# Kernel tuning notes

Measured on AMD Instinct MI355X. Metric: run time of the kernel, lower is better.

## Reference

```python
import jax, jax.numpy as jnp
import numpy as np

C_M = 256
C = 32
C_Z = 128
EPS = 1e-5


def setup_inputs() -> dict:
    key = jax.random.key(0)
    ks = jax.random.split(key, 8)
    b, s, i = 1, 128, 256
    msa = jax.random.normal(ks[0], (b, s, i, C_M), dtype=jnp.float32)
    scale_in = 1.0 / np.sqrt(C_M)
    scale_out = 1.0 / np.sqrt(C * C)
    return {
        "msa_representation": msa,
        "ln_w": jnp.ones((C_M,), jnp.float32),
        "ln_b": jnp.zeros((C_M,), jnp.float32),
        "w_left": jax.random.normal(ks[1], (C_M, C), jnp.float32) * scale_in,
        "b_left": jax.random.normal(ks[2], (C,), jnp.float32) * scale_in,
        "w_right": jax.random.normal(ks[3], (C_M, C), jnp.float32) * scale_in,
        "b_right": jax.random.normal(ks[4], (C,), jnp.float32) * scale_in,
        "w_out": jax.random.normal(ks[5], (C * C, C_Z), jnp.float32) * scale_out,
        "b_out": jax.random.normal(ks[6], (C_Z,), jnp.float32) * scale_out,
    }


def reference(msa_representation, ln_w, ln_b, w_left, b_left, w_right, b_right, w_out, b_out):
    x = msa_representation
    # LayerNorm over c_m
    mu = jnp.mean(x, axis=-1, keepdims=True)
    var = jnp.mean(jnp.square(x - mu), axis=-1, keepdims=True)
    x = (x - mu) * jax.lax.rsqrt(var + EPS) * ln_w + ln_b
    # dual projections: [b, s, i, c]
    A = x @ w_left + b_left
    B = x @ w_right + b_right
    s_dim = x.shape[1]
    # outer product mean over MSA depth s: [b, i, j, c, c]
    outer = jnp.einsum('bsic,bsjd->bijcd', A, B) / s_dim
    b_, i_, j_ = outer.shape[0], outer.shape[1], outer.shape[2]
    flat = outer.reshape(b_, i_, j_, C * C)
    return flat @ w_out + b_out
```

## Files before the change

### kernel.cpp

```cpp
#include <hip/hip_runtime.h>

typedef __attribute__((ext_vector_type(8))) short short8;
typedef __attribute__((ext_vector_type(4))) float f32x4;

#define CM 256
#define CC 32
#define CZ 128
#define SDIM 128
#define IDIM 256

__device__ __forceinline__ unsigned short f2bf(float f) {
  union { float f; unsigned u; } v; v.f = f;
  unsigned r = v.u + 0x7fffu + ((v.u >> 16) & 1u);
  return (unsigned short)(r >> 16);
}
__device__ __forceinline__ unsigned pack_bf2(float a, float b) {
  union { float f; unsigned u; } x, y; x.f = a; y.f = b;
  return ((x.u + 0x8000u) >> 16) | ((y.u + 0x8000u) & 0xffff0000u);
}

__global__ void k_prep(const float* __restrict__ wl, const float* __restrict__ wr,
                       const float* __restrict__ wo,
                       unsigned short* __restrict__ wlrT, unsigned short* __restrict__ WF) {
  int t = blockIdx.x * 256 + threadIdx.x;
  if (t < 64 * 256) {
    int c = t >> 8, e = t & 255;
    float v = (c < CC) ? wl[e * CC + c] : wr[e * CC + (c - CC)];
    wlrT[c * 256 + e] = f2bf(v);
  } else {
    int t2 = t - 64 * 256;
    if (t2 < 8 * 32 * 64) {
      int zt = t2 >> 11, ks = (t2 >> 6) & 31, lane = t2 & 63;
      int ln = lane & 15, qd = lane >> 4;
      int z = zt * 16 + ln;
#pragma unroll
      for (int e = 0; e < 8; ++e) {
        int c = qd * 8 + e, d = ks;
        WF[(size_t)t2 * 8 + e] = f2bf(wo[(c * 32 + d) * CZ + z] * (1.0f / 128.0f));
      }
    }
  }
}

__global__ __launch_bounds__(512) void k_lnproj(
    const float* __restrict__ x, const float* __restrict__ lnw, const float* __restrict__ lnb,
    const float* __restrict__ bl, const float* __restrict__ br,
    const unsigned short* __restrict__ wlrT,
    unsigned short* __restrict__ A2, unsigned short* __restrict__ Bbuf) {
  extern __shared__ __align__(16) char lds[];
  unsigned short* xn = (unsigned short*)lds;
  unsigned short* sT = (unsigned short*)(lds + 67584);
  int tid = threadIdx.x;
  int lane = tid & 63, ww = tid >> 6;
  int qd = lane >> 4, ln = lane & 15;
  int i = blockIdx.x;

  for (int rr = 0; rr < 16; ++rr) {
    int s = ww * 16 + rr;
    float4 v = ((const float4*)(x + ((size_t)s * IDIM + i) * CM))[lane];
    float s1 = v.x + v.y + v.z + v.w;
    float s2 = v.x * v.x + v.y * v.y + v.z * v.z + v.w * v.w;
#pragma unroll
    for (int off = 32; off; off >>= 1) {
      s1 += __shfl_xor(s1, off);
      s2 += __shfl_xor(s2, off);
    }
    float mu = s1 * (1.0f / 256.0f);
    float var = s2 * (1.0f / 256.0f) - mu * mu;
    float rs = rsqrtf(var + 1e-5f);
    float4 w4 = ((const float4*)lnw)[lane];
    float4 b4 = ((const float4*)lnb)[lane];
    ushort4 h;
    h.x = f2bf((v.x - mu) * rs * w4.x + b4.x);
    h.y = f2bf((v.y - mu) * rs * w4.y + b4.y);
    h.z = f2bf((v.z - mu) * rs * w4.z + b4.z);
    h.w = f2bf((v.w - mu) * rs * w4.w + b4.w);
    *(ushort4*)&xn[s * 264 + lane * 4] = h;
  }
  __syncthreads();

  f32x4 acc[4];
#pragma unroll
  for (int nt = 0; nt < 4; ++nt) acc[nt] = (f32x4){0.f, 0.f, 0.f, 0.f};
#pragma unroll
  for (int ks = 0; ks < 8; ++ks) {
    short8 af = *(const short8*)&xn[(ww * 16 + ln) * 264 + ks * 32 + qd * 8];
#pragma unroll
    for (int nt = 0; nt < 4; ++nt) {
      short8 bf = *(const short8*)(wlrT + (nt * 16 + ln) * 256 + ks * 32 + qd * 8);
      acc[nt] = __builtin_amdgcn_mfma_f32_16x16x32_bf16(af, bf, acc[nt], 0, 0, 0);
    }
  }
#pragma unroll
  for (int nt = 0; nt < 4; ++nt) {
    int c64 = nt * 16 + ln;
    float bias = (c64 < CC) ? bl[c64] : br[c64 - CC];
    ushort4 h;
    h.x = f2bf(acc[nt][0] + bias);
    h.y = f2bf(acc[nt][1] + bias);
    h.z = f2bf(acc[nt][2] + bias);
    h.w = f2bf(acc[nt][3] + bias);
    *(ushort4*)&sT[c64 * 136 + ww * 16 + qd * 4] = h;
  }
  __syncthreads();

  {
    int rtloc = ww >> 2, ks4 = ww & 3;
    short8 v = *(const short8*)&sT[(rtloc * 16 + ln) * 136 + ks4 * 32 + qd * 8];
    *(short8*)(A2 + ((size_t)(((2 * i + rtloc) * 4 + ks4) * 64 + lane)) * 8) = v;
  }
  {
    int row = tid >> 4, ch = tid & 15;
    short8 v = *(const short8*)&sT[(CC + row) * 136 + ch * 8];
    *(short8*)(Bbuf + ((size_t)(i * CC + row)) * SDIM + ch * 8) = v;
  }
}

__global__ __launch_bounds__(1024) void k_main(
    const unsigned short* __restrict__ A2, const unsigned short* __restrict__ Bbuf,
    const unsigned short* __restrict__ WF, const float* __restrict__ bout,
    float* __restrict__ out) {
  extern __shared__ __align__(16) char lds[];
  unsigned short* sB = (unsigned short*)lds;
  unsigned short* sP = (unsigned short*)lds;
  float* redF = (float*)lds;
  int tid = threadIdx.x;
  int lane = tid & 63, ww = tid >> 6;
  int qd = lane >> 4, ln = lane & 15;
  int i0 = blockIdx.x * 8, j0 = blockIdx.y * 8;

#pragma unroll
  for (int t = 0; t < 4; ++t) {
    int idx = tid + t * 1024;
    int r = idx >> 4, ch = idx & 15;
    short8 v = *(const short8*)(Bbuf + (size_t)(j0 * CC + r) * SDIM + ch * 8);
    *(short8*)&sB[r * 136 + ch * 8] = v;
  }
  __syncthreads();

  int wy = ww >> 2, wx = ww & 3;
  f32x4 acc1[4][4];
#pragma unroll
  for (int a = 0; a < 4; ++a)
#pragma unroll
    for (int b = 0; b < 4; ++b) acc1[a][b] = (f32x4){0.f, 0.f, 0.f, 0.f};
#pragma unroll
  for (int ks = 0; ks < 4; ++ks) {
    short8 af[4];
#pragma unroll
    for (int ti = 0; ti < 4; ++ti)
      af[ti] = *(const short8*)(A2 + ((size_t)((i0 * 2 + wy * 4 + ti) * 4 + ks) * 64 + lane) * 8);
#pragma unroll
    for (int tj = 0; tj < 4; ++tj) {
      short8 bf = *(const short8*)&sB[(wx * 64 + tj * 16 + ln) * 136 + ks * 32 + qd * 8];
#pragma unroll
      for (int ti = 0; ti < 4; ++ti)
        acc1[ti][tj] = __builtin_amdgcn_mfma_f32_16x16x32_bf16(af[ti], bf, acc1[ti][tj], 0, 0, 0);
    }
  }
  __syncthreads();

#pragma unroll
  for (int ti = 0; ti < 4; ++ti) {
    int iloc = wy * 2 + (ti >> 1);
    int cbase = 16 * (ti & 1) + qd * 4;
    int cb = cbase >> 3;
#pragma unroll
    for (int tj = 0; tj < 4; ++tj) {
      int jloc = wx * 2 + (tj >> 1);
      int d = 16 * (tj & 1) + ln;
      int p = iloc * 8 + jloc;
      uint2 u;
      u.x = pack_bf2(acc1[ti][tj][0], acc1[ti][tj][1]);
      u.y = pack_bf2(acc1[ti][tj][2], acc1[ti][tj][3]);
      *(uint2*)&sP[p * 1032 + d * 32 + ((((d >> 1) & 3) ^ cb) * 8) + (cbase & 7)] = u;
    }
  }
  __syncthreads();

  int ztq = ww & 1, kq = ww >> 1;
  f32x4 acc2[4][4];
#pragma unroll
  for (int a = 0; a < 4; ++a)
#pragma unroll
    for (int b = 0; b < 4; ++b) acc2[a][b] = (f32x4){0.f, 0.f, 0.f, 0.f};
  if (ww < 8) {
#pragma unroll
    for (int cc = 0; cc < 8; ++cc) {
      int ks = kq * 8 + cc;
      short8 afr[4];
#pragma unroll
      for (int mt = 0; mt < 4; ++mt)
        afr[mt] = *(const short8*)&sP[(mt * 16 + ln) * 1032 + ks * 32 + ((((ks >> 1) & 3) ^ qd) * 8)];
#pragma unroll
      for (int z4 = 0; z4 < 4; ++z4) {
        int zt = ztq * 4 + z4;
        short8 bfr = *(const short8*)(WF + ((size_t)(zt * 32 + ks) * 64 + lane) * 8);
#pragma unroll
        for (int mt = 0; mt < 4; ++mt)
          acc2[z4][mt] = __builtin_amdgcn_mfma_f32_16x16x32_bf16(bfr, afr[mt], acc2[z4][mt], 0, 0, 0);
      }
    }
  }

  __syncthreads();
  if (ww < 8 && kq >= 2) {
    int s = (kq - 2) * 2 + ztq;
#pragma unroll
    for (int z4 = 0; z4 < 4; ++z4)
#pragma unroll
      for (int mt = 0; mt < 4; ++mt)
        *(f32x4*)&redF[(s * 64 + mt * 16 + ln) * 68 + z4 * 16 + qd * 4] = acc2[z4][mt];
  }
  __syncthreads();
  if (ww < 8 && kq < 2) {
    int s = kq * 2 + ztq;
#pragma unroll
    for (int z4 = 0; z4 < 4; ++z4)
#pragma unroll
      for (int mt = 0; mt < 4; ++mt)
        acc2[z4][mt] += *(const f32x4*)&redF[(s * 64 + mt * 16 + ln) * 68 + z4 * 16 + qd * 4];
  }
  __syncthreads();
  if (ww < 8 && kq == 1) {
#pragma unroll
    for (int z4 = 0; z4 < 4; ++z4)
#pragma unroll
      for (int mt = 0; mt < 4; ++mt)
        *(f32x4*)&redF[(ztq * 64 + mt * 16 + ln) * 68 + z4 * 16 + qd * 4] = acc2[z4][mt];
  }
  __syncthreads();
  if (ww < 8 && kq == 0) {
#pragma unroll
    for (int z4 = 0; z4 < 4; ++z4) {
      int z = (ztq * 4 + z4) * 16 + qd * 4;
      f32x4 bz = *(const f32x4*)(bout + z);
#pragma unroll
      for (int mt = 0; mt < 4; ++mt) {
        int p = mt * 16 + ln;
        f32x4 v = acc2[z4][mt] + *(const f32x4*)&redF[(ztq * 64 + p) * 68 + z4 * 16 + qd * 4] + bz;
        int i = i0 + (p >> 3), j = j0 + (p & 7);
        *(f32x4*)&out[((size_t)i * IDIM + j) * CZ + z] = v;
      }
    }
  }
}

extern "C" void kernel_launch(void* const* d_in, const int* in_sizes, int n_in,
                              void* d_out, int out_size, void* d_ws, size_t ws_size,
                              hipStream_t stream) {
  const float* msa = (const float*)d_in[0];
  const float* lnw = (const float*)d_in[1];
  const float* lnb = (const float*)d_in[2];
  const float* wl  = (const float*)d_in[3];
  const float* bl  = (const float*)d_in[4];
  const float* wr  = (const float*)d_in[5];
  const float* br  = (const float*)d_in[6];
  const float* wo  = (const float*)d_in[7];
  const float* bo  = (const float*)d_in[8];
  float* out = (float*)d_out;

  char* ws = (char*)d_ws;
  unsigned short* A2   = (unsigned short*)ws;
  unsigned short* Bbuf = (unsigned short*)(ws + (2u << 20));
  unsigned short* wlrT = (unsigned short*)(ws + (4u << 20));
  unsigned short* WF   = (unsigned short*)(ws + (4u << 20) + 32768);

  (void)hipFuncSetAttribute((const void*)k_lnproj,
                            hipFuncAttributeMaxDynamicSharedMemorySize, 84992);
  (void)hipFuncSetAttribute((const void*)k_main,
                            hipFuncAttributeMaxDynamicSharedMemorySize, 132096);

  k_prep<<<128, 256, 0, stream>>>(wl, wr, wo, wlrT, WF);
  k_lnproj<<<256, 512, 84992, stream>>>(msa, lnw, lnb, bl, br, wlrT, A2, Bbuf);
  k_main<<<dim3(32, 32), 1024, 132096, stream>>>(A2, Bbuf, WF, bo, out);
}
```

Baseline: 157.2 us.

## Split LN-projection over MSA halves, prefragment weights, use all waves in output GEMM

k_lnproj now launches a 256x2 grid of 256-thread blocks, each handling 64 MSA rows with static LDS. This doubles block count and cuts per-block LDS. The projection weights are pre-packed into MFMA fragment order so each lane loads one contiguous short8. In k_main, the output GEMM now spreads over all 16 waves (2 z-tiles each) instead of 8 waves with 4 z-tiles, and the split-K reduction uses a lane-contiguous LDS layout. The risk is more LDS reduction traffic per block and added register and sync pressure across 16 waves.

```diff
diff --git a/kernel.cpp b/kernel.cpp
--- a/kernel.cpp
+++ b/kernel.cpp
@@ -21,14 +21,21 @@
 
 __global__ void k_prep(const float* __restrict__ wl, const float* __restrict__ wr,
                        const float* __restrict__ wo,
-                       unsigned short* __restrict__ wlrT, unsigned short* __restrict__ WF) {
+                       unsigned short* __restrict__ wlrT2, unsigned short* __restrict__ WF) {
   int t = blockIdx.x * 256 + threadIdx.x;
-  if (t < 64 * 256) {
-    int c = t >> 8, e = t & 255;
-    float v = (c < CC) ? wl[e * CC + c] : wr[e * CC + (c - CC)];
-    wlrT[c * 256 + e] = f2bf(v);
+  if (t < 2048) {
+    int frag = t >> 6, lane = t & 63;
+    int nt = frag >> 3, ks = frag & 7;
+    int ln = lane & 15, qd = lane >> 4;
+    int c64 = nt * 16 + ln;
+#pragma unroll
+    for (int e = 0; e < 8; ++e) {
+      int cm = ks * 32 + qd * 8 + e;
+      float v = (c64 < CC) ? wl[cm * CC + c64] : wr[cm * CC + (c64 - CC)];
+      wlrT2[(size_t)t * 8 + e] = f2bf(v);
+    }
   } else {
-    int t2 = t - 64 * 256;
+    int t2 = t - 2048;
     if (t2 < 8 * 32 * 64) {
       int zt = t2 >> 11, ks = (t2 >> 6) & 31, lane = t2 & 63;
       int ln = lane & 15, qd = lane >> 4;
@@ -42,21 +49,21 @@
   }
 }
 
-__global__ __launch_bounds__(512) void k_lnproj(
+__global__ __launch_bounds__(256) void k_lnproj(
     const float* __restrict__ x, const float* __restrict__ lnw, const float* __restrict__ lnb,
     const float* __restrict__ bl, const float* __restrict__ br,
-    const unsigned short* __restrict__ wlrT,
+    const unsigned short* __restrict__ wlrT2,
     unsigned short* __restrict__ A2, unsigned short* __restrict__ Bbuf) {
-  extern __shared__ __align__(16) char lds[];
-  unsigned short* xn = (unsigned short*)lds;
-  unsigned short* sT = (unsigned short*)(lds + 67584);
+  __shared__ __align__(16) unsigned short xn[64][264];
+  __shared__ __align__(16) unsigned short sT[64][72];
   int tid = threadIdx.x;
   int lane = tid & 63, ww = tid >> 6;
   int qd = lane >> 4, ln = lane & 15;
-  int i = blockIdx.x;
+  int i = blockIdx.x, sh = blockIdx.y;
 
   for (int rr = 0; rr < 16; ++rr) {
-    int s = ww * 16 + rr;
+    int sl = ww * 16 + rr;
+    int s = sh * 64 + sl;
     float4 v = ((const float4*)(x + ((size_t)s * IDIM + i) * CM))[lane];
     float s1 = v.x + v.y + v.z + v.w;
     float s2 = v.x * v.x + v.y * v.y + v.z * v.z + v.w * v.w;
@@ -75,7 +82,7 @@
     h.y = f2bf((v.y - mu) * rs * w4.y + b4.y);
     h.z = f2bf((v.z - mu) * rs * w4.z + b4.z);
     h.w = f2bf((v.w - mu) * rs * w4.w + b4.w);
-    *(ushort4*)&xn[s * 264 + lane * 4] = h;
+    *(ushort4*)&xn[sl][lane * 4] = h;
   }
   __syncthreads();
 
@@ -84,10 +91,10 @@
   for (int nt = 0; nt < 4; ++nt) acc[nt] = (f32x4){0.f, 0.f, 0.f, 0.f};
 #pragma unroll
   for (int ks = 0; ks < 8; ++ks) {
-    short8 af = *(const short8*)&xn[(ww * 16 + ln) * 264 + ks * 32 + qd * 8];
+    short8 af = *(const short8*)&xn[ww * 16 + ln][ks * 32 + qd * 8];
 #pragma unroll
     for (int nt = 0; nt < 4; ++nt) {
-      short8 bf = *(const short8*)(wlrT + (nt * 16 + ln) * 256 + ks * 32 + qd * 8);
+      short8 bf = *(const short8*)(wlrT2 + ((size_t)((nt * 8 + ks) * 64 + lane)) * 8);
       acc[nt] = __builtin_amdgcn_mfma_f32_16x16x32_bf16(af, bf, acc[nt], 0, 0, 0);
     }
   }
@@ -100,19 +107,19 @@
     h.y = f2bf(acc[nt][1] + bias);
     h.z = f2bf(acc[nt][2] + bias);
     h.w = f2bf(acc[nt][3] + bias);
-    *(ushort4*)&sT[c64 * 136 + ww * 16 + qd * 4] = h;
+    *(ushort4*)&sT[c64][ww * 16 + qd * 4] = h;
   }
   __syncthreads();
 
   {
-    int rtloc = ww >> 2, ks4 = ww & 3;
-    short8 v = *(const short8*)&sT[(rtloc * 16 + ln) * 136 + ks4 * 32 + qd * 8];
-    *(short8*)(A2 + ((size_t)(((2 * i + rtloc) * 4 + ks4) * 64 + lane)) * 8) = v;
+    int rtloc = ww >> 1, ksl = ww & 1;
+    short8 v = *(const short8*)&sT[rtloc * 16 + ln][ksl * 32 + qd * 8];
+    *(short8*)(A2 + ((size_t)(((2 * i + rtloc) * 4 + (sh * 2 + ksl)) * 64 + lane)) * 8) = v;
   }
   {
-    int row = tid >> 4, ch = tid & 15;
-    short8 v = *(const short8*)&sT[(CC + row) * 136 + ch * 8];
-    *(short8*)(Bbuf + ((size_t)(i * CC + row)) * SDIM + ch * 8) = v;
+    int row = tid >> 3, ch = tid & 7;
+    short8 v = *(const short8*)&sT[CC + row][ch * 8];
+    *(short8*)(Bbuf + ((size_t)(i * CC + row)) * SDIM + sh * 64 + ch * 8) = v;
   }
 }
 
@@ -123,7 +130,7 @@
   extern __shared__ __align__(16) char lds[];
   unsigned short* sB = (unsigned short*)lds;
   unsigned short* sP = (unsigned short*)lds;
-  float* redF = (float*)lds;
+  float* redR = (float*)lds;
   int tid = threadIdx.x;
   int lane = tid & 63, ww = tid >> 6;
   int qd = lane >> 4, ln = lane & 15;
@@ -178,67 +185,68 @@
   }
   __syncthreads();
 
-  int ztq = ww & 1, kq = ww >> 1;
-  f32x4 acc2[4][4];
-#pragma unroll
-  for (int a = 0; a < 4; ++a)
+  int ztp = ww & 3, kq = ww >> 2;
+  f32x4 acc2[2][4];
+#pragma unroll
+  for (int a = 0; a < 2; ++a)
 #pragma unroll
     for (int b = 0; b < 4; ++b) acc2[a][b] = (f32x4){0.f, 0.f, 0.f, 0.f};
-  if (ww < 8) {
-#pragma unroll
-    for (int cc = 0; cc < 8; ++cc) {
-      int ks = kq * 8 + cc;
-      short8 afr[4];
-#pragma unroll
-      for (int mt = 0; mt < 4; ++mt)
-        afr[mt] = *(const short8*)&sP[(mt * 16 + ln) * 1032 + ks * 32 + ((((ks >> 1) & 3) ^ qd) * 8)];
-#pragma unroll
-      for (int z4 = 0; z4 < 4; ++z4) {
-        int zt = ztq * 4 + z4;
-        short8 bfr = *(const short8*)(WF + ((size_t)(zt * 32 + ks) * 64 + lane) * 8);
-#pragma unroll
-        for (int mt = 0; mt < 4; ++mt)
-          acc2[z4][mt] = __builtin_amdgcn_mfma_f32_16x16x32_bf16(bfr, afr[mt], acc2[z4][mt], 0, 0, 0);
-      }
-    }
-  }
-
-  __syncthreads();
-  if (ww < 8 && kq >= 2) {
-    int s = (kq - 2) * 2 + ztq;
-#pragma unroll
-    for (int z4 = 0; z4 < 4; ++z4)
-#pragma unroll
-      for (int mt = 0; mt < 4; ++mt)
-        *(f32x4*)&redF[(s * 64 + mt * 16 + ln) * 68 + z4 * 16 + qd * 4] = acc2[z4][mt];
-  }
-  __syncthreads();
-  if (ww < 8 && kq < 2) {
-    int s = kq * 2 + ztq;
-#pragma unroll
-    for (int z4 = 0; z4 < 4; ++z4)
-#pragma unroll
-      for (int mt = 0; mt < 4; ++mt)
-        acc2[z4][mt] += *(const f32x4*)&redF[(s * 64 + mt * 16 + ln) * 68 + z4 * 16 + qd * 4];
-  }
-  __syncthreads();
-  if (ww < 8 && kq == 1) {
-#pragma unroll
-    for (int z4 = 0; z4 < 4; ++z4)
-#pragma unroll
-      for (int mt = 0; mt < 4; ++mt)
-        *(f32x4*)&redF[(ztq * 64 + mt * 16 + ln) * 68 + z4 * 16 + qd * 4] = acc2[z4][mt];
-  }
-  __syncthreads();
-  if (ww < 8 && kq == 0) {
-#pragma unroll
-    for (int z4 = 0; z4 < 4; ++z4) {
-      int z = (ztq * 4 + z4) * 16 + qd * 4;
+#pragma unroll
+  for (int cc = 0; cc < 8; ++cc) {
+    int ks = kq * 8 + cc;
+    short8 afr[4];
+#pragma unroll
+    for (int mt = 0; mt < 4; ++mt)
+      afr[mt] = *(const short8*)&sP[(mt * 16 + ln) * 1032 + ks * 32 + ((((ks >> 1) & 3) ^ qd) * 8)];
+#pragma unroll
+    for (int h2 = 0; h2 < 2; ++h2) {
+      int zt = ztp * 2 + h2;
+      short8 bfr = *(const short8*)(WF + ((size_t)(zt * 32 + ks) * 64 + lane) * 8);
+#pragma unroll
+      for (int mt = 0; mt < 4; ++mt)
+        acc2[h2][mt] = __builtin_amdgcn_mfma_f32_16x16x32_bf16(bfr, afr[mt], acc2[h2][mt], 0, 0, 0);
+    }
+  }
+
+  __syncthreads();
+  if (kq >= 2) {
+    int s = (kq - 2) * 4 + ztp;
+#pragma unroll
+    for (int h2 = 0; h2 < 2; ++h2)
+#pragma unroll
+      for (int mt = 0; mt < 4; ++mt)
+        *(f32x4*)&redR[(((s * 2 + h2) * 4 + mt) << 8) + lane * 4] = acc2[h2][mt];
+  }
+  __syncthreads();
+  if (kq < 2) {
+    int s = kq * 4 + ztp;
+#pragma unroll
+    for (int h2 = 0; h2 < 2; ++h2)
+#pragma unroll
+      for (int mt = 0; mt < 4; ++mt)
+        acc2[h2][mt] += *(const f32x4*)&redR[(((s * 2 + h2) * 4 + mt) << 8) + lane * 4];
+  }
+  __syncthreads();
+  if (kq == 1) {
+    int s = ztp;
+#pragma unroll
+    for (int h2 = 0; h2 < 2; ++h2)
+#pragma unroll
+      for (int mt = 0; mt < 4; ++mt)
+        *(f32x4*)&redR[(((s * 2 + h2) * 4 + mt) << 8) + lane * 4] = acc2[h2][mt];
+  }
+  __syncthreads();
+  if (kq == 0) {
+    int s = ztp;
+#pragma unroll
+    for (int h2 = 0; h2 < 2; ++h2) {
+      int z = (ztp * 2 + h2) * 16 + qd * 4;
       f32x4 bz = *(const f32x4*)(bout + z);
 #pragma unroll
       for (int mt = 0; mt < 4; ++mt) {
         int p = mt * 16 + ln;
-        f32x4 v = acc2[z4][mt] + *(const f32x4*)&redF[(ztq * 64 + p) * 68 + z4 * 16 + qd * 4] + bz;
+        f32x4 v = acc2[h2][mt] +
+                  *(const f32x4*)&redR[(((s * 2 + h2) * 4 + mt) << 8) + lane * 4] + bz;
         int i = i0 + (p >> 3), j = j0 + (p & 7);
         *(f32x4*)&out[((size_t)i * IDIM + j) * CZ + z] = v;
       }
@@ -261,17 +269,15 @@
   float* out = (float*)d_out;
 
   char* ws = (char*)d_ws;
-  unsigned short* A2   = (unsigned short*)ws;
-  unsigned short* Bbuf = (unsigned short*)(ws + (2u << 20));
-  unsigned short* wlrT = (unsigned short*)(ws + (4u << 20));
-  unsigned short* WF   = (unsigned short*)(ws + (4u << 20) + 32768);
-
-  (void)hipFuncSetAttribute((const void*)k_lnproj,
-                            hipFuncAttributeMaxDynamicSharedMemorySize, 84992);
+  unsigned short* A2    = (unsigned short*)ws;
+  unsigned short* Bbuf  = (unsigned short*)(ws + (2u << 20));
+  unsigned short* wlrT2 = (unsigned short*)(ws + (4u << 20));
+  unsigned short* WF    = (unsigned short*)(ws + (4u << 20) + 32768);
+
   (void)hipFuncSetAttribute((const void*)k_main,
                             hipFuncAttributeMaxDynamicSharedMemorySize, 132096);
 
-  k_prep<<<128, 256, 0, stream>>>(wl, wr, wo, wlrT, WF);
-  k_lnproj<<<256, 512, 84992, stream>>>(msa, lnw, lnb, bl, br, wlrT, A2, Bbuf);
+  k_prep<<<72, 256, 0, stream>>>(wl, wr, wo, wlrT2, WF);
+  k_lnproj<<<dim3(256, 2), 256, 0, stream>>>(msa, lnw, lnb, bl, br, wlrT2, A2, Bbuf);
   k_main<<<dim3(32, 32), 1024, 132096, stream>>>(A2, Bbuf, WF, bo, out);
 }
```

After: 141.6 us. -9.9%, faster.
